# Performance work log

Measured on AMD Instinct MI355X. Metric: run time of the kernel, lower is better.

Reference implementation:

```python
import jax, jax.numpy as jnp
import numpy as np

D = 128   # num_variables
H = 16    # hidden_dim
B = 8192  # batch size


def setup_inputs() -> dict:
    key = jax.random.key(0)
    ks = jax.random.split(key, 8)
    X = jax.random.normal(ks[0], (B, D), dtype=jnp.float32)
    adjacency_logits = jax.random.normal(ks[1], (D, D), dtype=jnp.float32) * 0.1
    temperature = jnp.array(1.0, dtype=jnp.float32)
    # Fixed Gumbel noise for F.gumbel_softmax (deterministic reference)
    u = jax.random.uniform(ks[2], (D, D, 2), dtype=jnp.float32, minval=1e-6, maxval=1.0 - 1e-6)
    gumbel = -jnp.log(-jnp.log(u))
    # Stacked per-variable MLP params (torch Linear default init: U(-1/sqrt(fan_in), 1/sqrt(fan_in)))
    lim1 = 1.0 / np.sqrt(D)
    lim2 = 1.0 / np.sqrt(H)
    W1 = jax.random.uniform(ks[3], (D, D, H), dtype=jnp.float32, minval=-lim1, maxval=lim1)  # [var, in, hid]
    b1 = jax.random.uniform(ks[4], (D, H), dtype=jnp.float32, minval=-lim1, maxval=lim1)
    W2 = jax.random.uniform(ks[5], (D, H), dtype=jnp.float32, minval=-lim2, maxval=lim2)     # [var, hid] (out dim 1)
    b2 = jax.random.uniform(ks[6], (D,), dtype=jnp.float32, minval=-lim2, maxval=lim2)
    return {"X": X, "adjacency_logits": adjacency_logits, "temperature": temperature,
            "gumbel": gumbel, "W1": W1, "b1": b1, "W2": W2, "b2": b2}


def _soft_adjacency(adjacency_logits, temperature, gumbel):
    # binary gumbel-softmax over {off, on}, take P(on), zero the diagonal
    logits2 = jnp.stack([-adjacency_logits, adjacency_logits], axis=-1)  # [D, D, 2]
    y = jax.nn.softmax((logits2 + gumbel) / temperature, axis=-1)
    A = y[..., 1] * (1.0 - jnp.eye(adjacency_logits.shape[0], dtype=adjacency_logits.dtype))
    return A


def reference(X, adjacency_logits, temperature, gumbel, W1, b1, W2, b2):
    A = _soft_adjacency(adjacency_logits, temperature, gumbel)  # [D, D], A[v, i] = edge v->i
    # masked input for variable i: X * A[:, i]  ->  masked[b, i, v] = X[b, v] * A[v, i]
    masked = X[:, None, :] * A.T[None, :, :]                    # [B, D, D]
    hidden = jax.nn.relu(jnp.einsum('biv,ivh->bih', masked, W1) + b1)  # [B, D, H]
    recon = jnp.einsum('bih,ih->bi', hidden, W2) + b2            # [B, D]
    return recon, A
```

## Files before the change

kernel.cpp:

```cpp
#include <hip/hip_runtime.h>
#include <hip/hip_fp16.h>

#define DD 128
#define HH 16
#define BB 8192

typedef _Float16 hf8 __attribute__((ext_vector_type(8)));
typedef _Float16 hf4 __attribute__((ext_vector_type(4)));
typedef _Float16 hf2 __attribute__((ext_vector_type(2)));
typedef float f32x4 __attribute__((ext_vector_type(4)));

static __device__ __forceinline__ hf2 pkrtz(float a, float b) {
    return __builtin_bit_cast(hf2, __builtin_amdgcn_cvt_pkrtz(a, b));
}

__global__ void k_prep(const float* __restrict__ L, const float* __restrict__ Tptr,
                       const float* __restrict__ g, const float* __restrict__ W1,
                       float* __restrict__ Aout, _Float16* __restrict__ Wt) {
    int idx = blockIdx.x * blockDim.x + threadIdx.x;
    int v = idx & (DD - 1);
    int h = (idx >> 7) & (HH - 1);
    int i = idx >> 11;
    int vi = v * DD + i;
    float t = Tptr[0];
    float z = (2.0f * L[vi] + g[2 * vi + 1] - g[2 * vi]) / t;
    float a = 1.0f / (1.0f + __expf(-z));
    if (v == i) a = 0.0f;
    if (h == 0) Aout[vi] = a;
    Wt[idx] = (_Float16)(a * W1[(i * DD + v) * HH + h]);
}

__launch_bounds__(128)
__global__ void k_main(const float* __restrict__ X, const _Float16* __restrict__ Wt,
                       const float* __restrict__ b1, const float* __restrict__ W2,
                       const float* __restrict__ b2, float* __restrict__ out) {
    const int tid  = threadIdx.x;
    const int wave = tid >> 6;
    const int lane = tid & 63;
    const int m    = lane & 15;
    const int q    = lane >> 4;

    const int b0 = blockIdx.x * 128 + wave * 64;
    const int i0 = blockIdx.y * 16;

    hf8 xb[4][4];
#pragma unroll
    for (int t = 0; t < 4; t++) {
        const float* xp = X + (size_t)(b0 + t * 16 + m) * DD + q * 8;
#pragma unroll
        for (int s = 0; s < 4; s++) {
            f32x4 lo = *(const f32x4*)(xp + s * 32);
            f32x4 hi = *(const f32x4*)(xp + s * 32 + 4);
            hf2 p0 = pkrtz(lo[0], lo[1]);
            hf2 p1 = pkrtz(lo[2], lo[3]);
            hf2 p2 = pkrtz(hi[0], hi[1]);
            hf2 p3 = pkrtz(hi[2], hi[3]);
            hf4 l4 = __builtin_shufflevector(p0, p1, 0, 1, 2, 3);
            hf4 h4 = __builtin_shufflevector(p2, p3, 0, 1, 2, 3);
            xb[t][s] = __builtin_shufflevector(l4, h4, 0, 1, 2, 3, 4, 5, 6, 7);
        }
    }

    f32x4 w2f = *(const f32x4*)(W2 + (i0 + m) * HH + q * 4);
    hf2 wlo = pkrtz(w2f[0], w2f[1]);
    hf2 whi = pkrtz(w2f[2], w2f[3]);
    hf4 w2self = __builtin_shufflevector(wlo, whi, 0, 1, 2, 3);
    const hf4 hzero = {(_Float16)0.f, (_Float16)0.f, (_Float16)0.f, (_Float16)0.f};

    const float b2v = b2[i0 + m];
    f32x4 acc2[4];
#pragma unroll
    for (int t = 0; t < 4; t++) acc2[t] = (f32x4){b2v, b2v, b2v, b2v};

#pragma unroll 2
    for (int ii = 0; ii < 16; ii++) {
        const int i = i0 + ii;
        const _Float16* wp = Wt + (i * HH + m) * DD + q * 8;
        f32x4 b1v = *(const f32x4*)(b1 + i * HH + q * 4);
        f32x4 a[4] = {b1v, b1v, b1v, b1v};
#pragma unroll
        for (int s = 0; s < 4; s++) {
            hf8 wa = *(const hf8*)(wp + s * 32);
#pragma unroll
            for (int t = 0; t < 4; t++)
                a[t] = __builtin_amdgcn_mfma_f32_16x16x32_f16(wa, xb[t][s], a[t], 0, 0, 0);
        }
        hf4 bfrag = (m == ii) ? w2self : hzero;
#pragma unroll
        for (int t = 0; t < 4; t++) {
            hf2 plo = pkrtz(__builtin_fmaxf(a[t][0], 0.f),
                            __builtin_fmaxf(a[t][1], 0.f));
            hf2 phi = pkrtz(__builtin_fmaxf(a[t][2], 0.f),
                            __builtin_fmaxf(a[t][3], 0.f));
            hf4 p = __builtin_shufflevector(plo, phi, 0, 1, 2, 3);
            acc2[t] = __builtin_amdgcn_mfma_f32_16x16x16f16(p, bfrag, acc2[t], 0, 0, 0);
        }
    }

#pragma unroll
    for (int t = 0; t < 4; t++)
#pragma unroll
        for (int r = 0; r < 4; r++)
            out[(size_t)(b0 + t * 16 + q * 4 + r) * DD + i0 + m] = acc2[t][r];
}

extern "C" void kernel_launch(void* const* d_in, const int* in_sizes, int n_in,
                              void* d_out, int out_size, void* d_ws, size_t ws_size,
                              hipStream_t stream) {
    const float* X  = (const float*)d_in[0];
    const float* L  = (const float*)d_in[1];
    const float* T  = (const float*)d_in[2];
    const float* g  = (const float*)d_in[3];
    const float* W1 = (const float*)d_in[4];
    const float* b1 = (const float*)d_in[5];
    const float* W2 = (const float*)d_in[6];
    const float* b2 = (const float*)d_in[7];

    float* recon = (float*)d_out;
    float* Aout  = recon + (size_t)BB * DD;

    _Float16* Wt = (_Float16*)d_ws;

    k_prep<<<(DD * HH * DD) / 256, 256, 0, stream>>>(L, T, g, W1, Aout, Wt);

    dim3 grid(BB / 128, DD / 16);
    k_main<<<grid, 128, 0, stream>>>(X, Wt, b1, W2, b2, recon);
}
```

Baseline: 90.94 us.

## Fuse adjacency prep into main kernel with swizzled LDS weight tiles

Removes the separate prep kernel and its global fp16 weight workspace. Each block now recomputes the Gumbel-sigmoid adjacency and the masked fp16 W1 slice for its 16 output variables, and stages them in 64KB of XOR-swizzled shared memory that the MFMA loop reads. This drops one launch and the global round trip of the prepared weights. In exchange every block redundantly recomputes and rereads W1 from global (64x redundancy), and the 64KB LDS allocation limits occupancy.

```diff
diff --git a/kernel.cpp b/kernel.cpp
--- a/kernel.cpp
+++ b/kernel.cpp
@@ -9,31 +9,20 @@
 typedef _Float16 hf4 __attribute__((ext_vector_type(4)));
 typedef _Float16 hf2 __attribute__((ext_vector_type(2)));
 typedef float f32x4 __attribute__((ext_vector_type(4)));
+typedef float f32x2 __attribute__((ext_vector_type(2)));
 
 static __device__ __forceinline__ hf2 pkrtz(float a, float b) {
     return __builtin_bit_cast(hf2, __builtin_amdgcn_cvt_pkrtz(a, b));
 }
 
-__global__ void k_prep(const float* __restrict__ L, const float* __restrict__ Tptr,
-                       const float* __restrict__ g, const float* __restrict__ W1,
-                       float* __restrict__ Aout, _Float16* __restrict__ Wt) {
-    int idx = blockIdx.x * blockDim.x + threadIdx.x;
-    int v = idx & (DD - 1);
-    int h = (idx >> 7) & (HH - 1);
-    int i = idx >> 11;
-    int vi = v * DD + i;
-    float t = Tptr[0];
-    float z = (2.0f * L[vi] + g[2 * vi + 1] - g[2 * vi]) / t;
-    float a = 1.0f / (1.0f + __expf(-z));
-    if (v == i) a = 0.0f;
-    if (h == 0) Aout[vi] = a;
-    Wt[idx] = (_Float16)(a * W1[(i * DD + v) * HH + h]);
-}
+__launch_bounds__(128)
+__global__ void k_fused(const float* __restrict__ X, const float* __restrict__ L,
+                        const float* __restrict__ Tptr, const float* __restrict__ g,
+                        const float* __restrict__ W1, const float* __restrict__ b1,
+                        const float* __restrict__ W2, const float* __restrict__ b2,
+                        float* __restrict__ out, float* __restrict__ Aout) {
+    extern __shared__ _Float16 wt[];
 
-__launch_bounds__(128)
-__global__ void k_main(const float* __restrict__ X, const _Float16* __restrict__ Wt,
-                       const float* __restrict__ b1, const float* __restrict__ W2,
-                       const float* __restrict__ b2, float* __restrict__ out) {
     const int tid  = threadIdx.x;
     const int wave = tid >> 6;
     const int lane = tid & 63;
@@ -61,26 +50,63 @@
         }
     }
 
+    const float tinv = 1.0f / Tptr[0];
+    const int v0 = lane * 2;
+#pragma unroll 2
+    for (int kk = 0; kk < 8; kk++) {
+        const int il = wave * 8 + kk;
+        const int i  = i0 + il;
+        const int vi0 = v0 * DD + i;
+        const int vi1 = vi0 + DD;
+        f32x2 g0 = *(const f32x2*)(g + 2 * (size_t)vi0);
+        f32x2 g1 = *(const f32x2*)(g + 2 * (size_t)vi1);
+        float z0 = (2.0f * L[vi0] + g0[1] - g0[0]) * tinv;
+        float z1 = (2.0f * L[vi1] + g1[1] - g1[0]) * tinv;
+        float a0 = 1.0f / (1.0f + __expf(-z0));
+        float a1 = 1.0f / (1.0f + __expf(-z1));
+        if (v0 == i)     a0 = 0.0f;
+        if (v0 + 1 == i) a1 = 0.0f;
+        if (blockIdx.x == 0) { Aout[vi0] = a0; Aout[vi1] = a1; }
+        const float* w1p = W1 + ((size_t)i * DD + v0) * HH;
+        f32x4 wva[4], wvb[4];
+#pragma unroll
+        for (int s = 0; s < 4; s++) wva[s] = *(const f32x4*)(w1p + 4 * s);
+#pragma unroll
+        for (int s = 0; s < 4; s++) wvb[s] = *(const f32x4*)(w1p + HH + 4 * s);
+        char* rowp = (char*)wt + il * (HH * 256);
+        const int cb = 4 * lane;
+#pragma unroll
+        for (int h = 0; h < HH; h++) {
+            hf2 val;
+            val[0] = (_Float16)(a0 * wva[h >> 2][h & 3]);
+            val[1] = (_Float16)(a1 * wvb[h >> 2][h & 3]);
+            *(hf2*)(rowp + h * 256 + (cb ^ ((h & 7) << 4))) = val;
+        }
+    }
+
     f32x4 w2f = *(const f32x4*)(W2 + (i0 + m) * HH + q * 4);
     hf2 wlo = pkrtz(w2f[0], w2f[1]);
     hf2 whi = pkrtz(w2f[2], w2f[3]);
     hf4 w2self = __builtin_shufflevector(wlo, whi, 0, 1, 2, 3);
     const hf4 hzero = {(_Float16)0.f, (_Float16)0.f, (_Float16)0.f, (_Float16)0.f};
-
     const float b2v = b2[i0 + m];
     f32x4 acc2[4];
 #pragma unroll
     for (int t = 0; t < 4; t++) acc2[t] = (f32x4){b2v, b2v, b2v, b2v};
 
+    __syncthreads();
+
+    const char* wbase = (const char*)wt + m * 256;
+    const int swz = (m & 7) << 4;
 #pragma unroll 2
     for (int ii = 0; ii < 16; ii++) {
         const int i = i0 + ii;
-        const _Float16* wp = Wt + (i * HH + m) * DD + q * 8;
+        const char* rp = wbase + ii * (HH * 256);
         f32x4 b1v = *(const f32x4*)(b1 + i * HH + q * 4);
         f32x4 a[4] = {b1v, b1v, b1v, b1v};
 #pragma unroll
         for (int s = 0; s < 4; s++) {
-            hf8 wa = *(const hf8*)(wp + s * 32);
+            hf8 wa = *(const hf8*)(rp + ((s * 64 + q * 16) ^ swz));
 #pragma unroll
             for (int t = 0; t < 4; t++)
                 a[t] = __builtin_amdgcn_mfma_f32_16x16x32_f16(wa, xb[t][s], a[t], 0, 0, 0);
@@ -119,10 +145,8 @@
     float* recon = (float*)d_out;
     float* Aout  = recon + (size_t)BB * DD;
 
-    _Float16* Wt = (_Float16*)d_ws;
-
-    k_prep<<<(DD * HH * DD) / 256, 256, 0, stream>>>(L, T, g, W1, Aout, Wt);
+    (void)d_ws; (void)ws_size;
 
     dim3 grid(BB / 128, DD / 16);
-    k_main<<<grid, 128, 0, stream>>>(X, Wt, b1, W2, b2, recon);
+    k_fused<<<grid, 128, 65536, stream>>>(X, L, T, g, W1, b1, W2, b2, recon, Aout);
 }
```

Result: slower. 93.47 us (+2.8%).

## Double-buffer weight fragments in main loop and vectorize prep kernel per (i,v)

Applied to the files above, without the earlier changes.

The main kernel now preloads all b1 vectors and double-buffers the Wt MFMA fragments, loading the next variable's weights while computing the current one, so global-load latency overlaps with MFMA work. The prep kernel is restructured so each thread handles one (i,v) pair, computing the sigmoid once and reading 16 W1 values with vector loads instead of one thread per (i,h,v). Launch bounds add a minimum of two blocks per SIMD/CU. The cost is higher register pressure from the extra buffers, and the prep kernel's stores become strided across h.

```diff
diff --git a/kernel.cpp b/kernel.cpp
--- a/kernel.cpp
+++ b/kernel.cpp
@@ -9,6 +9,7 @@
 typedef _Float16 hf4 __attribute__((ext_vector_type(4)));
 typedef _Float16 hf2 __attribute__((ext_vector_type(2)));
 typedef float f32x4 __attribute__((ext_vector_type(4)));
+typedef float f32x2 __attribute__((ext_vector_type(2)));
 
 static __device__ __forceinline__ hf2 pkrtz(float a, float b) {
     return __builtin_bit_cast(hf2, __builtin_amdgcn_cvt_pkrtz(a, b));
@@ -17,20 +18,26 @@
 __global__ void k_prep(const float* __restrict__ L, const float* __restrict__ Tptr,
                        const float* __restrict__ g, const float* __restrict__ W1,
                        float* __restrict__ Aout, _Float16* __restrict__ Wt) {
-    int idx = blockIdx.x * blockDim.x + threadIdx.x;
-    int v = idx & (DD - 1);
-    int h = (idx >> 7) & (HH - 1);
-    int i = idx >> 11;
+    int gid = blockIdx.x * 64 + threadIdx.x;
+    int v = gid & (DD - 1);
+    int i = gid >> 7;
     int vi = v * DD + i;
     float t = Tptr[0];
-    float z = (2.0f * L[vi] + g[2 * vi + 1] - g[2 * vi]) / t;
+    f32x2 gg = *(const f32x2*)(g + 2 * (size_t)vi);
+    float z = (2.0f * L[vi] + gg[1] - gg[0]) / t;
     float a = 1.0f / (1.0f + __expf(-z));
     if (v == i) a = 0.0f;
-    if (h == 0) Aout[vi] = a;
-    Wt[idx] = (_Float16)(a * W1[(i * DD + v) * HH + h]);
+    Aout[vi] = a;
+    const float* w1p = W1 + ((size_t)i * DD + v) * HH;
+    f32x4 w[4];
+#pragma unroll
+    for (int s = 0; s < 4; s++) w[s] = *(const f32x4*)(w1p + 4 * s);
+#pragma unroll
+    for (int h = 0; h < HH; h++)
+        Wt[i * (HH * DD) + h * DD + v] = (_Float16)(a * w[h >> 2][h & 3]);
 }
 
-__launch_bounds__(128)
+__launch_bounds__(128, 2)
 __global__ void k_main(const float* __restrict__ X, const _Float16* __restrict__ Wt,
                        const float* __restrict__ b1, const float* __restrict__ W2,
                        const float* __restrict__ b2, float* __restrict__ out) {
@@ -72,30 +79,50 @@
 #pragma unroll
     for (int t = 0; t < 4; t++) acc2[t] = (f32x4){b2v, b2v, b2v, b2v};
 
-#pragma unroll 2
-    for (int ii = 0; ii < 16; ii++) {
-        const int i = i0 + ii;
-        const _Float16* wp = Wt + (i * HH + m) * DD + q * 8;
-        f32x4 b1v = *(const f32x4*)(b1 + i * HH + q * 4);
-        f32x4 a[4] = {b1v, b1v, b1v, b1v};
+    f32x4 b1all[16];
 #pragma unroll
-        for (int s = 0; s < 4; s++) {
-            hf8 wa = *(const hf8*)(wp + s * 32);
+    for (int ii = 0; ii < 16; ii++)
+        b1all[ii] = *(const f32x4*)(b1 + (i0 + ii) * HH + q * 4);
+
+    const _Float16* wbase = Wt + ((size_t)i0 * HH + m) * DD + q * 8;
+
+    hf8 wa0[4], wa1[4];
 #pragma unroll
-            for (int t = 0; t < 4; t++)
-                a[t] = __builtin_amdgcn_mfma_f32_16x16x32_f16(wa, xb[t][s], a[t], 0, 0, 0);
-        }
-        hf4 bfrag = (m == ii) ? w2self : hzero;
+    for (int s = 0; s < 4; s++) wa0[s] = *(const hf8*)(wbase + s * 32);
+
+#define STEP(IIC, WUSE, WPRE, PRE_II)                                          \
+    {                                                                          \
+        if ((PRE_II) < 16) {                                                   \
+            const _Float16* np = wbase + (size_t)(PRE_II) * (HH * DD);         \
+            _Pragma("unroll")                                                  \
+            for (int s = 0; s < 4; s++) WPRE[s] = *(const hf8*)(np + s * 32);  \
+        }                                                                      \
+        f32x4 b1v = b1all[(IIC)];                                              \
+        f32x4 a[4] = {b1v, b1v, b1v, b1v};                                     \
+        _Pragma("unroll")                                                      \
+        for (int s = 0; s < 4; s++) {                                          \
+            _Pragma("unroll")                                                  \
+            for (int t = 0; t < 4; t++)                                        \
+                a[t] = __builtin_amdgcn_mfma_f32_16x16x32_f16(WUSE[s], xb[t][s], a[t], 0, 0, 0); \
+        }                                                                      \
+        hf4 bfrag = (m == (IIC)) ? w2self : hzero;                             \
+        _Pragma("unroll")                                                      \
+        for (int t = 0; t < 4; t++) {                                          \
+            hf2 plo = pkrtz(__builtin_fmaxf(a[t][0], 0.f),                     \
+                            __builtin_fmaxf(a[t][1], 0.f));                    \
+            hf2 phi = pkrtz(__builtin_fmaxf(a[t][2], 0.f),                     \
+                            __builtin_fmaxf(a[t][3], 0.f));                    \
+            hf4 p = __builtin_shufflevector(plo, phi, 0, 1, 2, 3);             \
+            acc2[t] = __builtin_amdgcn_mfma_f32_16x16x16f16(p, bfrag, acc2[t], 0, 0, 0); \
+        }                                                                      \
+    }
+
 #pragma unroll
-        for (int t = 0; t < 4; t++) {
-            hf2 plo = pkrtz(__builtin_fmaxf(a[t][0], 0.f),
-                            __builtin_fmaxf(a[t][1], 0.f));
-            hf2 phi = pkrtz(__builtin_fmaxf(a[t][2], 0.f),
-                            __builtin_fmaxf(a[t][3], 0.f));
-            hf4 p = __builtin_shufflevector(plo, phi, 0, 1, 2, 3);
-            acc2[t] = __builtin_amdgcn_mfma_f32_16x16x16f16(p, bfrag, acc2[t], 0, 0, 0);
-        }
+    for (int jj = 0; jj < 8; jj++) {
+        STEP(2 * jj,     wa0, wa1, 2 * jj + 1);
+        STEP(2 * jj + 1, wa1, wa0, 2 * jj + 2);
     }
+#undef STEP
 
 #pragma unroll
     for (int t = 0; t < 4; t++)
@@ -121,7 +148,7 @@
 
     _Float16* Wt = (_Float16*)d_ws;
 
-    k_prep<<<(DD * HH * DD) / 256, 256, 0, stream>>>(L, T, g, W1, Aout, Wt);
+    k_prep<<<(DD * DD) / 64, 64, 0, stream>>>(L, T, g, W1, Aout, Wt);
 
     dim3 grid(BB / 128, DD / 16);
     k_main<<<grid, 128, 0, stream>>>(X, Wt, b1, W2, b2, recon);
```

New measurement: 85.60 us. 5.9% less time.
